# Optimization experiments

Measured on AMD Instinct MI355X. Metric: run time of the kernel, lower is better.

## Reference

```python
import jax, jax.numpy as jnp
import numpy as np

B, S, HID = 1, 2048, 2048
NH = 16
QL, KVL = 1536, 512
DN, DR, DV = 128, 64, 128
DQ = DN + DR  # 192
IH, ID = 4, 128
TOPK = 1024
EPS = 1e-6
THETA = 10000.0


def rope_interleaved(x, cos, sin):
    # x: (b,s,h,d); cos/sin: (s,d//2); pairs are (x[...,2i], x[...,2i+1])
    xr = x[..., 0::2]
    xi = x[..., 1::2]
    c = cos[None, :, None, :]
    s = sin[None, :, None, :]
    yr = xr * c - xi * s
    yi = xr * s + xi * c
    return jnp.stack([yr, yi], axis=-1).reshape(x.shape)


def rope_noninterleaved(x, cos, sin):
    # rotate-half style: pairs are (x[...,i], x[...,i+d/2])
    d = x.shape[-1] // 2
    x1, x2 = x[..., :d], x[..., d:]
    c = cos[None, :, None, :]
    s = sin[None, :, None, :]
    return jnp.concatenate([x1 * c - x2 * s, x1 * s + x2 * c], axis=-1)


def rmsnorm(x, w):
    var = jnp.mean(x * x, axis=-1, keepdims=True)
    return w * (x * jax.lax.rsqrt(var + EPS))


def layernorm(x, g, b):
    mu = jnp.mean(x, axis=-1, keepdims=True)
    var = jnp.mean((x - mu) ** 2, axis=-1, keepdims=True)
    return (x - mu) * jax.lax.rsqrt(var + EPS) * g + b


def setup_inputs() -> dict:
    key = jax.random.key(0)
    ks = jax.random.split(key, 12)
    std = 0.02
    x = jax.random.normal(ks[0], (B, S, HID), jnp.float32)
    pos = jnp.arange(S, dtype=jnp.float32)
    inv_freq = THETA ** (-jnp.arange(0, DR, 2, dtype=jnp.float32) / DR)
    ang = pos[:, None] * inv_freq[None, :]  # (S, DR//2)
    cos, sin = jnp.cos(ang), jnp.sin(ang)
    mask = jnp.where(jnp.tril(jnp.ones((S, S), bool)), 0.0, -1e9).astype(jnp.float32)
    return {
        "x": x, "cos": cos, "sin": sin, "mask": mask,
        "Wq_a": jax.random.normal(ks[1], (HID, QL), jnp.float32) * std,
        "q_norm_w": jnp.ones((QL,), jnp.float32),
        "Wq_b": jax.random.normal(ks[2], (QL, NH * DQ), jnp.float32) * std,
        "Wkv_a": jax.random.normal(ks[3], (HID, KVL + DR), jnp.float32) * std,
        "kv_norm_w": jnp.ones((KVL,), jnp.float32),
        "Wkv_b": jax.random.normal(ks[4], (KVL, NH * (DN + DV)), jnp.float32) * std,
        "Wo": jax.random.normal(ks[5], (NH * DV, HID), jnp.float32) * std,
        "IWq_b": jax.random.normal(ks[6], (QL, IH * ID), jnp.float32) * std,
        "IWk": jax.random.normal(ks[7], (HID, ID), jnp.float32) * std,
        "Ik_norm_w": jnp.ones((ID,), jnp.float32),
        "Ik_norm_b": jnp.zeros((ID,), jnp.float32),
        "IWproj": jax.random.normal(ks[8], (HID, IH), jnp.float32) * std,
    }


def indexer(x, qr, cos, sin, mask, IWq_b, IWk, Ik_norm_w, Ik_norm_b, IWproj):
    b, s, _ = x.shape
    q = (qr @ IWq_b).reshape(b, s, IH, ID)
    q_pe, q_nope = q[..., :DR], q[..., DR:]
    q_pe = rope_noninterleaved(q_pe, cos, sin)
    q = jnp.concatenate([q_pe, q_nope], axis=-1)
    k = layernorm(x @ IWk, Ik_norm_w, Ik_norm_b)  # (b,s,ID)
    k_pe = rope_noninterleaved(k[:, :, None, :DR], cos, sin)[:, :, 0]
    k = jnp.concatenate([k_pe, k[..., DR:]], axis=-1)
    weights = (x @ IWproj) * (IH ** -0.5) * (ID ** -0.5)  # (b,s,IH)
    logits = jax.nn.relu(jnp.einsum('bthd,bsd->btsh', q, k))
    index_score = jnp.einsum('btsh,bth->bts', logits, weights)
    index_score = index_score + mask[None]
    k_top = min(TOPK, s)
    topk_idx = jax.lax.top_k(index_score, k_top)[1]  # (b,s,k)
    bi = jnp.arange(b)[:, None, None]
    si = jnp.arange(s)[None, :, None]
    index_mask = jnp.full((b, s, s), -1e9, jnp.float32).at[bi, si, topk_idx].set(0.0)
    return index_mask


def reference(x, cos, sin, mask, Wq_a, q_norm_w, Wq_b, Wkv_a, kv_norm_w, Wkv_b, Wo,
              IWq_b, IWk, Ik_norm_w, Ik_norm_b, IWproj):
    b, s, _ = x.shape
    qr = rmsnorm(x @ Wq_a, q_norm_w)  # (b,s,QL)
    q = (qr @ Wq_b).reshape(b, s, NH, DQ)
    q_nope, q_pe = q[..., :DN], q[..., DN:]
    q_pe = rope_interleaved(q_pe, cos, sin)
    q = jnp.concatenate([q_nope, q_pe], axis=-1)
    kv_full = x @ Wkv_a
    kv, k_pe = kv_full[..., :KVL], kv_full[..., KVL:]
    kv = rmsnorm(kv, kv_norm_w)
    k_pe = rope_interleaved(k_pe[:, :, None, :], cos, sin)  # (b,s,1,DR)
    kv_exp = (kv @ Wkv_b).reshape(b, s, NH, DN + DV)
    k_nope, v = kv_exp[..., :DN], kv_exp[..., DN:]
    k = jnp.concatenate([k_nope, jnp.broadcast_to(k_pe, (b, s, NH, DR))], axis=-1)
    scores = jnp.einsum('bshd,bthd->bsht', q, k) * (DQ ** -0.5)
    index_mask = indexer(x, qr, cos, sin, mask, IWq_b, IWk, Ik_norm_w, Ik_norm_b, IWproj)
    scores = scores + index_mask[:, :, None, :] + mask[None, :, None, :]
    probs = jax.nn.softmax(scores, axis=-1)
    out = jnp.einsum('bsht,bthd->bshd', probs, v).reshape(b, s, NH * DV)
    return out @ Wo
```

## Files before the change

kernel.cpp:

```cpp
#include <hip/hip_runtime.h>
#include <math.h>
#include <stdint.h>

#define S 2048
#define HID 2048
#define NH 16
#define QL 1536
#define KVL 512
#define DN 128
#define DR 64
#define DV 128
#define DQ 192
#define IH 4
#define ID 128
#define TOPK 1024

#define N1 2244
#define N2 3584

#define WT_OFF3 ((size_t)N2 * QL)
#define WT_OFF4 (WT_OFF3 + (size_t)4096 * KVL)
#define WT_OFF5 (WT_OFF4 + (size_t)2048 * 2048)
#define WT_TOTAL (WT_OFF5 + (size_t)N1 * HID)

#define CDIV(a,b) (((a)+(b)-1)/(b))

typedef float f32x4 __attribute__((ext_vector_type(4)));
typedef short bf16x8 __attribute__((ext_vector_type(8)));

__device__ __forceinline__ ushort f2b(float f) {
    uint32_t u = __float_as_uint(f);
    u += 0x7fffu + ((u >> 16) & 1u);
    return (ushort)(u >> 16);
}

#define GLL16(g, l)                                                            \
    __builtin_amdgcn_global_load_lds(                                          \
        (const __attribute__((address_space(1))) void*)(g),                    \
        (__attribute__((address_space(3))) void*)(l), 16, 0, 0)

#define STG64T(k0, s)                                                          \
    {                                                                          \
        _Pragma("unroll")                                                      \
        for (int p = 0; p < 4; p++) {                                          \
            GLL16(pA[p] + (k0), As + (s) * 8192 + p * 2048 + doff);            \
            GLL16(pB[p] + (k0), Bs + (s) * 8192 + p * 2048 + doff);            \
        }                                                                      \
    }

template<int HALF>
__device__ __forceinline__ void gemm_tile(const ushort* __restrict__ A,
                                          const ushort* __restrict__ BT,
                                          void* __restrict__ Cv,
                                          int N, int K, int row0, int col0,
                                          ushort* As, ushort* Bs) {
    const int tid = threadIdx.x;
    const int w = tid >> 6, l = tid & 63;
    const int quad = l >> 4, lane = l & 15;
    const int wr = (w >> 1) * 64, wc = (w & 1) * 64;
    f32x4 acc[4][4];
#pragma unroll
    for (int i = 0; i < 4; i++)
#pragma unroll
        for (int j = 0; j < 4; j++) acc[i][j] = (f32x4)0.f;

    const int r32 = tid >> 3;
    const int csw = (((tid & 7) ^ (r32 & 7)) * 8);
    const ushort* pA[4];
    const ushort* pB[4];
#pragma unroll
    for (int p = 0; p < 4; p++) {
        pA[p] = A + (size_t)(row0 + p * 32 + r32) * K + csw;
        int bn = col0 + p * 32 + r32; if (bn > N - 1) bn = N - 1;
        pB[p] = BT + (size_t)bn * K + csw;
    }
    const int doff = r32 * 64 + (tid & 7) * 8;

    const int nt = K >> 6;
    STG64T(0, 0);
    asm volatile("s_waitcnt vmcnt(0)" ::: "memory");
    __builtin_amdgcn_s_barrier();

    const int xsw = (lane & 7) << 3;
    int cur = 0;
    for (int t = 0; t < nt; ++t) {
        if (t + 1 < nt) STG64T((t + 1) * 64, cur ^ 1);
#pragma unroll
        for (int kk = 0; kk < 2; kk++) {
            const int fo = (kk * 32 + quad * 8) ^ xsw;
            bf16x8 af[4], bf[4];
#pragma unroll
            for (int mi = 0; mi < 4; mi++)
                af[mi] = *(const bf16x8*)(As + cur * 8192 + (wr + mi * 16 + lane) * 64 + fo);
#pragma unroll
            for (int ni = 0; ni < 4; ni++)
                bf[ni] = *(const bf16x8*)(Bs + cur * 8192 + (wc + ni * 16 + lane) * 64 + fo);
#pragma unroll
            for (int mi = 0; mi < 4; mi++)
#pragma unroll
                for (int ni = 0; ni < 4; ni++)
                    acc[mi][ni] = __builtin_amdgcn_mfma_f32_16x16x32_bf16(af[mi], bf[ni], acc[mi][ni], 0, 0, 0);
        }
        asm volatile("s_waitcnt vmcnt(0)" ::: "memory");
        __builtin_amdgcn_s_barrier();
        cur ^= 1;
    }
#pragma unroll
    for (int mi = 0; mi < 4; mi++)
#pragma unroll
        for (int ni = 0; ni < 4; ni++)
#pragma unroll
            for (int r = 0; r < 4; r++) {
                int row = row0 + wr + mi * 16 + quad * 4 + r;
                int col = col0 + wc + ni * 16 + lane;
                if (col < N) {
                    if (HALF) ((ushort*)Cv)[(size_t)row * N + col] = f2b(acc[mi][ni][r]);
                    else      ((float*)Cv)[(size_t)row * N + col] = acc[mi][ni][r];
                }
            }
}

__device__ __forceinline__ void wtrans_lds(const float* W, ushort* WT, int K, int N,
                                           int k0, int n0, float* t) {
    int rr = threadIdx.x >> 6, cc = threadIdx.x & 63;
#pragma unroll
    for (int p = 0; p < 16; p++) {
        int k = k0 + p * 4 + rr, n = n0 + cc;
        t[(p * 4 + rr) * 65 + cc] = (k < K && n < N) ? W[(size_t)k * N + n] : 0.f;
    }
    __syncthreads();
#pragma unroll
    for (int p = 0; p < 16; p++) {
        int n = n0 + p * 4 + rr, k = k0 + cc;
        if (n < N && k < K) WT[(size_t)n * K + k] = f2b(t[cc * 65 + p * 4 + rr]);
    }
}

__global__ __launch_bounds__(256) void prep1(const float* __restrict__ x,
                                             ushort* __restrict__ xb,
                                             const float* __restrict__ W0,
                                             const float* __restrict__ W1,
                                             const float* __restrict__ W2,
                                             const float* __restrict__ W3,
                                             ushort* __restrict__ WTc1) {
    __shared__ float tb[64 * 65];
    const int id = blockIdx.x;
    if (id < 1152) {
        const float* W; int N; size_t off; int loc;
        if (id < 768)       { W = W0; N = 1536; off = 0;                  loc = id; }
        else if (id < 1056) { W = W1; N = 576;  off = (size_t)1536 * HID; loc = id - 768; }
        else if (id < 1120) { W = W2; N = 128;  off = (size_t)2112 * HID; loc = id - 1056; }
        else                { W = W3; N = 4;    off = (size_t)2240 * HID; loc = id - 1120; }
        wtrans_lds(W, WTc1 + off, HID, N, (loc & 31) * 64, (loc >> 5) * 64, tb);
    } else {
        const int i = (id - 1152) * 256 + threadIdx.x;
        float4 v = *(const float4*)(x + (size_t)i * 4);
        uint32_t lo = (uint32_t)f2b(v.x) | ((uint32_t)f2b(v.y) << 16);
        uint32_t hi = (uint32_t)f2b(v.z) | ((uint32_t)f2b(v.w) << 16);
        *(uint2*)(xb + (size_t)i * 4) = make_uint2(lo, hi);
    }
}

__global__ __launch_bounds__(256) void prep2(const float* __restrict__ W0,
                                             const float* __restrict__ W1,
                                             const float* __restrict__ Wkvb,
                                             const float* __restrict__ Wo,
                                             ushort* __restrict__ WT) {
    __shared__ float tb[64 * 65];
    const int id = blockIdx.x;
    const float* W; int K, N, nx; size_t off; int loc;
    if (id < 1152)      { W = W0;   K = QL;   N = 3072; nx = 24; off = 0;                 loc = id; }
    else if (id < 1344) { W = W1;   K = QL;   N = 512;  nx = 24; off = (size_t)3072 * QL; loc = id - 1152; }
    else if (id < 1856) { W = Wkvb; K = KVL;  N = 4096; nx = 8;  off = WT_OFF3;           loc = id - 1344; }
    else                { W = Wo;   K = 2048; N = 2048; nx = 32; off = WT_OFF4;           loc = id - 1856; }
    wtrans_lds(W, WT + off, K, N, (loc % nx) * 64, (loc / nx) * 64, tb);
}

__global__ __launch_bounds__(256) void gemm_f32(const ushort* __restrict__ A,
                                                const ushort* __restrict__ BT,
                                                float* __restrict__ C,
                                                int N, int K) {
    __shared__ ushort As[2][8192];
    __shared__ ushort Bs[2][8192];
    gemm_tile<0>(A, BT, C, N, K, blockIdx.y * 128, blockIdx.x * 128,
                 &As[0][0], &Bs[0][0]);
}

__global__ __launch_bounds__(256) void megaC2(const ushort* __restrict__ qrb,
                                              const ushort* __restrict__ kvnb,
                                              const ushort* __restrict__ WT,
                                              float* __restrict__ C2,
                                              ushort* __restrict__ kvexp_h) {
    __shared__ ushort As[2][8192];
    __shared__ ushort Bs[2][8192];
    const int id = blockIdx.x;
    if (id < 448) {
        gemm_tile<0>(qrb, WT, C2, N2, QL, (id / 28) * 128, (id % 28) * 128,
                     &As[0][0], &Bs[0][0]);
    } else {
        const int loc = id - 448;
        gemm_tile<1>(kvnb, WT + WT_OFF3, kvexp_h, 4096, KVL,
                     (loc / 32) * 128, (loc % 32) * 128, &As[0][0], &Bs[0][0]);
    }
}

__global__ __launch_bounds__(256) void post_c1(const float* __restrict__ C1,
                                               const float* __restrict__ qw,
                                               const float* __restrict__ kvw,
                                               const float* __restrict__ ikg,
                                               const float* __restrict__ ikb,
                                               const float* __restrict__ cosb,
                                               const float* __restrict__ sinb,
                                               ushort* __restrict__ qrb,
                                               ushort* __restrict__ kvnb,
                                               float* __restrict__ kpe,
                                               float* __restrict__ kiT) {
    const int t = blockIdx.x, tid = threadIdx.x;
    const float* row = C1 + (size_t)t * N1;
    __shared__ float red[256];
    __shared__ float kis[128];
    float ss = 0.f;
    for (int i = tid; i < 1536; i += 256) { float v = row[i]; ss += v * v; }
    red[tid] = ss; __syncthreads();
    for (int st = 128; st > 0; st >>= 1) { if (tid < st) red[tid] += red[tid + st]; __syncthreads(); }
    float sq = rsqrtf(red[0] / 1536.f + 1e-6f);
    __syncthreads();
    float s2 = 0.f;
    for (int i = tid; i < 512; i += 256) { float v = row[1536 + i]; s2 += v * v; }
    red[tid] = s2; __syncthreads();
    for (int st = 128; st > 0; st >>= 1) { if (tid < st) red[tid] += red[tid + st]; __syncthreads(); }
    float skv = rsqrtf(red[0] / 512.f + 1e-6f);
    __syncthreads();
    float kv_ = (tid < 128) ? row[2112 + tid] : 0.f;
    red[tid] = kv_; __syncthreads();
    for (int st = 128; st > 0; st >>= 1) { if (tid < st) red[tid] += red[tid + st]; __syncthreads(); }
    float mu = red[0] / 128.f;
    __syncthreads();
    red[tid] = kv_ * kv_; __syncthreads();
    for (int st = 128; st > 0; st >>= 1) { if (tid < st) red[tid] += red[tid + st]; __syncthreads(); }
    float var = red[0] / 128.f - mu * mu;
    for (int i = tid; i < 1536; i += 256) qrb[(size_t)t * QL + i] = f2b(row[i] * sq * qw[i]);
    for (int i = tid; i < 512; i += 256)  kvnb[(size_t)t * KVL + i] = f2b(row[1536 + i] * skv * kvw[i]);
    if (tid < 32) {
        float c = cosb[t * 32 + tid], s = sinb[t * 32 + tid];
        float xr = row[2048 + 2 * tid], xi = row[2048 + 2 * tid + 1];
        kpe[t * 64 + 2 * tid]     = xr * c - xi * s;
        kpe[t * 64 + 2 * tid + 1] = xr * s + xi * c;
    }
    if (tid < 128) kis[tid] = (kv_ - mu) * rsqrtf(var + 1e-6f) * ikg[tid] + ikb[tid];
    __syncthreads();
    if (tid < 128) {
        float outv;
        if (tid < 32) {
            float c = cosb[t * 32 + tid], s = sinb[t * 32 + tid];
            outv = kis[tid] * c - kis[tid + 32] * s;
        } else if (tid < 64) {
            int j = tid - 32;
            float c = cosb[t * 32 + j], s = sinb[t * 32 + j];
            outv = kis[j] * s + kis[tid] * c;
        } else {
            outv = kis[tid];
        }
        kiT[(size_t)tid * S + t] = outv;
    }
}

__global__ __launch_bounds__(256) void megaPost(float* __restrict__ C2,
                                                const float* __restrict__ cosb,
                                                const float* __restrict__ sinb,
                                                ushort* __restrict__ qb,
                                                const ushort* __restrict__ kvexp_h,
                                                const float* __restrict__ kpe,
                                                ushort* __restrict__ kb,
                                                ushort* __restrict__ vT) {
    __shared__ float cs[32], sn[32];
    __shared__ ushort tt[64][136];
    const int id = blockIdx.x, tid = threadIdx.x;
    if (id < 2048) {
        const int t = id;
        if (tid < 32) { cs[tid] = cosb[t * 32 + tid]; sn[tid] = sinb[t * 32 + tid]; }
        __syncthreads();
        const float sc = 0.10412775370051047f;
        const float* src0 = C2 + (size_t)t * N2;
        for (int i = tid; i < NH * 96; i += 256) {
            int h = i / 96, p = i % 96;
            const float* src = src0 + h * 192;
            ushort* dst = qb + ((size_t)h * S + t) * 192;
            if (p < 64) {
                dst[2 * p]     = f2b(src[2 * p] * sc);
                dst[2 * p + 1] = f2b(src[2 * p + 1] * sc);
            } else {
                int j = p - 64;
                float c = cs[j], s = sn[j];
                float xr = src[128 + 2 * j], xi = src[128 + 2 * j + 1];
                dst[128 + 2 * j]     = f2b((xr * c - xi * s) * sc);
                dst[128 + 2 * j + 1] = f2b((xr * s + xi * c) * sc);
            }
        }
        if (tid < 128) {
            int h = tid >> 5, j = tid & 31;
            float* p = C2 + (size_t)t * N2 + 3072 + h * 128;
            float c = cs[j], s = sn[j];
            float x1 = p[j], x2 = p[j + 32];
            p[j] = x1 * c - x2 * s;
            p[j + 32] = x1 * s + x2 * c;
        }
    } else {
        const int loc = id - 2048;
        const int s0 = (loc & 31) * 64, h = loc >> 5;
        const int row = tid >> 2, c = tid & 3;
        const ushort* src = kvexp_h + (size_t)(s0 + row) * 4096 + h * 256;
        ushort* kbr = kb + ((size_t)h * S + s0 + row) * 192;
#pragma unroll
        for (int i = 0; i < 4; i++) {
            int off = c * 32 + i * 8;
            *(uint4*)(kbr + off) = *(const uint4*)(src + off);
            *(uint4*)(&tt[row][off]) = *(const uint4*)(src + 128 + off);
        }
        const float* kp = kpe + (size_t)(s0 + row) * 64 + c * 16;
#pragma unroll
        for (int i = 0; i < 16; i++) kbr[128 + c * 16 + i] = f2b(kp[i]);
        __syncthreads();
        const int d = tid >> 1, sh = (tid & 1) * 32;
        ushort* dst = vT + ((size_t)h * 128 + d) * S + s0 + sh;
#pragma unroll
        for (int i = 0; i < 32; i++) dst[i] = tt[sh + i][d];
    }
}

__global__ __launch_bounds__(256) void iscore4x4(const float* __restrict__ qi,
                                                 const float* __restrict__ kiT,
                                                 const float* __restrict__ iw,
                                                 float* __restrict__ iscore) {
    const int t0 = blockIdx.x * 4;
    const int s0 = blockIdx.y * 1024;
    if (s0 > t0 + 3) return;
    const int s = s0 + threadIdx.x * 4;
    __shared__ float qsT[4 * ID * 4];
    __shared__ float ws[16];
    for (int i = threadIdx.x; i < 4 * ID * 4; i += 256) {
        int tt = i & 3, hd = i >> 2;
        qsT[hd * 4 + tt] = qi[(size_t)(t0 + tt) * N2 + hd];
    }
    if (threadIdx.x < 16) {
        int tt = threadIdx.x >> 2, h = threadIdx.x & 3;
        ws[threadIdx.x] = iw[(size_t)(t0 + tt) * N1 + h] * 0.04419417382415922f;
    }
    __syncthreads();
    if (s > t0 + 3) return;
    float a[4][4][4];
#pragma unroll
    for (int tt = 0; tt < 4; tt++)
#pragma unroll
        for (int h = 0; h < 4; h++)
#pragma unroll
            for (int c = 0; c < 4; c++) a[tt][h][c] = 0.f;
    for (int d = 0; d < ID; d++) {
        float4 kv = *(const float4*)(kiT + (size_t)d * S + s);
#pragma unroll
        for (int h = 0; h < 4; h++) {
            float4 qv = *(const float4*)(&qsT[(h * ID + d) * 4]);
            a[0][h][0] += qv.x * kv.x; a[0][h][1] += qv.x * kv.y;
            a[0][h][2] += qv.x * kv.z; a[0][h][3] += qv.x * kv.w;
            a[1][h][0] += qv.y * kv.x; a[1][h][1] += qv.y * kv.y;
            a[1][h][2] += qv.y * kv.z; a[1][h][3] += qv.y * kv.w;
            a[2][h][0] += qv.z * kv.x; a[2][h][1] += qv.z * kv.y;
            a[2][h][2] += qv.z * kv.z; a[2][h][3] += qv.z * kv.w;
            a[3][h][0] += qv.w * kv.x; a[3][h][1] += qv.w * kv.y;
            a[3][h][2] += qv.w * kv.z; a[3][h][3] += qv.w * kv.w;
        }
    }
#pragma unroll
    for (int tt = 0; tt < 4; tt++) {
        const int t = t0 + tt;
        if (s > t) continue;
#pragma unroll
        for (int c = 0; c < 4; c++) {
            if (s + c > t) break;
            float sc = fmaxf(a[tt][0][c], 0.f) * ws[tt * 4 + 0] +
                       fmaxf(a[tt][1][c], 0.f) * ws[tt * 4 + 1] +
                       fmaxf(a[tt][2][c], 0.f) * ws[tt * 4 + 2] +
                       fmaxf(a[tt][3][c], 0.f) * ws[tt * 4 + 3];
            iscore[(size_t)t * S + s + c] = sc;
        }
    }
}

__device__ inline unsigned sortable_u32(float f) {
    unsigned u = __float_as_uint(f);
    return (u & 0x80000000u) ? ~u : (u | 0x80000000u);
}

__global__ __launch_bounds__(256) void topk_mask(const float* __restrict__ iscore,
                                                 uint32_t* __restrict__ msk) {
    int t = blockIdx.x, tid = threadIdx.x;
    uint32_t* mrow = msk + (size_t)t * 64;
    if (t < TOPK) {
        if (tid < 64) {
            int full = (t + 1) >> 5;
            uint32_t wv2 = (tid < full) ? 0xFFFFFFFFu : 0u;
            if (tid == full) { int rem = (t + 1) & 31; wv2 = rem ? ((1u << rem) - 1u) : 0u; }
            mrow[tid] = wv2;
        }
        return;
    }
    const float* row = iscore + (size_t)t * S;
    const int n = t + 1;
    const int wv = tid >> 6, lane = tid & 63;
    __shared__ int hist[4][256];
    __shared__ int wtot[4];
    __shared__ int bsel, ksel;
    __shared__ uint32_t bytes[256];

    int jb = tid * 8;
    float4 v0 = *(const float4*)(row + jb);
    float4 v1 = *(const float4*)(row + jb + 4);
    uint32_t lsu[8];
    {
        float vvv[8] = {v0.x, v0.y, v0.z, v0.w, v1.x, v1.y, v1.z, v1.w};
#pragma unroll
        for (int i = 0; i < 8; i++)
            lsu[i] = (jb + i < n) ? sortable_u32(vvv[i]) : 0u;
    }
    unsigned prefix = 0, prefmask = 0;
    int k = TOPK;
    for (int pass = 0; pass < 4; pass++) {
        int shift = 24 - pass * 8;
#pragma unroll
        for (int r = 0; r < 4; r++) hist[r][tid] = 0;
        __syncthreads();
#pragma unroll
        for (int i = 0; i < 8; i++) {
            uint32_t u = lsu[i];
            if ((u & prefmask) == prefix) atomicAdd(&hist[wv][(u >> shift) & 255], 1);
        }
        __syncthreads();
        int h = hist[0][tid] + hist[1][tid] + hist[2][tid] + hist[3][tid];
        int x = h;
#pragma unroll
        for (int off = 1; off < 64; off <<= 1) {
            int tmp = __shfl_down(x, off, 64);
            if (lane + off < 64) x += tmp;
        }
        if (lane == 0) wtot[wv] = x;
        __syncthreads();
        int add = 0;
#pragma unroll
        for (int w2 = 1; w2 < 4; w2++) if (w2 > wv) add += wtot[w2];
        x += add;
        int snext = x - h;
        if (x >= k && snext < k) { bsel = tid; ksel = k - snext; }
        __syncthreads();
        prefix |= ((unsigned)bsel) << shift;
        prefmask |= 0xFFu << shift;
        k = ksel;
        __syncthreads();
    }
    const unsigned u_thr = prefix;
    const int need = k;
    uint32_t gtbits = 0, eqbits = 0;
    int eqcnt = 0;
#pragma unroll
    for (int i = 0; i < 8; i++) {
        uint32_t u = lsu[i];
        if (u > u_thr) gtbits |= 1u << i;
        else if (u == u_thr) { eqbits |= 1u << i; eqcnt++; }
    }
    {
        int x = eqcnt;
#pragma unroll
        for (int off = 1; off < 64; off <<= 1) {
            int tmp = __shfl_up(x, off, 64);
            if (lane >= off) x += tmp;
        }
        if (lane == 63) wtot[wv] = x;
        __syncthreads();
        int add = 0;
#pragma unroll
        for (int w2 = 0; w2 < 3; w2++) if (w2 < wv) add += wtot[w2];
        x += add;
        int room = need - (x - eqcnt);
        uint32_t keep = 0;
#pragma unroll
        for (int i = 0; i < 8; i++)
            if ((eqbits >> i) & 1u) { if (room > 0) { keep |= 1u << i; room--; } }
        bytes[tid] = gtbits | keep;
    }
    __syncthreads();
    if (tid < 64)
        mrow[tid] = bytes[tid * 4] | (bytes[tid * 4 + 1] << 8) |
                    (bytes[tid * 4 + 2] << 16) | (bytes[tid * 4 + 3] << 24);
}

__global__ __launch_bounds__(256, 2) void fattn10(const ushort* __restrict__ qb,
                                                  const ushort* __restrict__ kb,
                                                  const ushort* __restrict__ vT,
                                                  const uint32_t* __restrict__ msk,
                                                  float* __restrict__ Opart,
                                                  float* __restrict__ mlbuf) {
    __shared__ ushort Ks[24 * 512];
    __shared__ ushort Vs[16 * 512];
    __shared__ ushort Pm[4][16 * 72];
    const int tid = threadIdx.x;
    const int w = tid >> 6, l = tid & 63, quad = l >> 4, lane = l & 15;
    const int b = blockIdx.x;
    const int r8 = b & 7, j = b >> 3;
    const int h = r8 + 8 * (j & 1);
    const int idx = j >> 1;
    const int pair = idx & 15, part = idx >> 4;
    const int ta = pair, tb = 31 - pair, nA = ta + 1;
    const int vlo = part * 11, vhi = vlo + 11;
    const int qa0 = ta * 64, qb0 = tb * 64;

    bf16x8 qfa[6], qfb[6];
    {
        const ushort* qpa = qb + ((size_t)h * S + qa0 + w * 16 + lane) * 192;
        const ushort* qpb = qb + ((size_t)h * S + qb0 + w * 16 + lane) * 192;
#pragma unroll
        for (int ks = 0; ks < 6; ks++) {
            qfa[ks] = *(const bf16x8*)(qpa + ks * 32 + quad * 8);
            qfb[ks] = *(const bf16x8*)(qpb + ks * 32 + quad * 8);
        }
    }
    f32x4 oa[8], ob[8];
#pragma unroll
    for (int i = 0; i < 8; i++) { oa[i] = (f32x4)0.f; ob[i] = (f32x4)0.f; }
    float la[4], lb[4];
#pragma unroll
    for (int r = 0; r < 4; r++) { la[r] = 0.f; lb[r] = 0.f; }

    ushort* pw = &Pm[w][0];
    const ushort* kbase = kb + (size_t)h * S * 192;
    const ushort* vbase = vT + (size_t)h * 128 * S;

    for (int kt = 0; kt <= tb; kt++) {
        const int idxB = (kt <= ta) ? 2 * kt : kt + nA;
        const int hasA = (kt <= ta);
        const int idxA = 2 * kt + 1;
        const bool doB = (idxB >= vlo && idxB < vhi);
        const bool doA = hasA && (idxA >= vlo && idxA < vhi);
        if (!(doA || doB)) continue;
        const int s0 = kt * 64;
        __syncthreads();
#pragma unroll
        for (int ii = 0; ii < 6; ii++) {
            const int i = w * 6 + ii;
            const int ks = i >> 2, kq = i & 3;
            const ushort* src = kbase + (size_t)(s0 + kq * 16 + lane) * 192 + ks * 32 + quad * 8;
            GLL16(src, Ks + i * 512 + l * 8);
        }
#pragma unroll
        for (int ii = 0; ii < 4; ii++) {
            const int i = w * 4 + ii;
            const int k2 = i >> 3, nt = i & 7;
            const ushort* src = vbase + (size_t)(nt * 16 + lane) * S + s0 + k2 * 32 + quad * 8;
            GLL16(src, Vs + i * 512 + l * 8);
        }
        __syncthreads();

#pragma unroll
        for (int pass = 0; pass < 2; pass++) {
            if (pass == 0 && !doA) continue;
            if (pass == 1 && !doB) continue;
            const bf16x8* qf = (pass == 0) ? qfa : qfb;
            f32x4* oacc      = (pass == 0) ? oa : ob;
            float* ll        = (pass == 0) ? la : lb;
            const int q0t    = (pass == 0) ? qa0 : qb0;

            f32x4 sc[4];
#pragma unroll
            for (int kq = 0; kq < 4; kq++) {
                sc[kq] = (f32x4)0.f;
#pragma unroll
                for (int ks = 0; ks < 6; ks++) {
                    bf16x8 bfr = *(const bf16x8*)(Ks + (ks * 4 + kq) * 512 + quad * 128 + lane * 8);
                    sc[kq] = __builtin_amdgcn_mfma_f32_16x16x32_bf16(qf[ks], bfr, sc[kq], 0, 0, 0);
                }
            }
            uint32_t w0[4], w1[4];
            {
                const int rowbase = q0t + w * 16 + quad * 4;
#pragma unroll
                for (int r = 0; r < 4; r++) {
                    const uint32_t* mp = msk + (size_t)(rowbase + r) * 64 + (s0 >> 5);
                    w0[r] = mp[0]; w1[r] = mp[1];
                }
            }
#pragma unroll
            for (int kq = 0; kq < 4; kq++) {
                const int sh = (kq & 1) * 16 + lane;
#pragma unroll
                for (int r = 0; r < 4; r++) {
                    uint32_t word = (kq < 2) ? w0[r] : w1[r];
                    float v = ((word >> sh) & 1u) ? sc[kq][r] : -1e30f;
                    float e = exp2f(v);
                    ll[r] += e;
                    pw[(quad * 4 + r) * 72 + kq * 16 + lane] = f2b(e);
                }
            }

            bf16x8 pfr[2];
#pragma unroll
            for (int k2 = 0; k2 < 2; k2++)
                pfr[k2] = *(const bf16x8*)(pw + lane * 72 + k2 * 32 + quad * 8);
#pragma unroll
            for (int nt = 0; nt < 8; nt++) {
#pragma unroll
                for (int k2 = 0; k2 < 2; k2++) {
                    bf16x8 vfr = *(const bf16x8*)(Vs + ((k2 * 8 + nt) * 4 + quad) * 128 + lane * 8);
                    oacc[nt] = __builtin_amdgcn_mfma_f32_16x16x32_bf16(pfr[k2], vfr, oacc[nt], 0, 0, 0);
                }
            }
        }
    }
#pragma unroll
    for (int off = 1; off < 16; off <<= 1)
#pragma unroll
        for (int r = 0; r < 4; r++) {
            la[r] += __shfl_xor(la[r], off, 64);
            lb[r] += __shfl_xor(lb[r], off, 64);
        }
#pragma unroll
    for (int pass = 0; pass < 2; pass++) {
        const f32x4* oacc = (pass == 0) ? oa : ob;
        const float* ll   = (pass == 0) ? la : lb;
        const int qt      = (pass == 0) ? ta : tb;
        float* Op = Opart + (size_t)((qt * 16 + h) * 3 + part) * (64 * 128);
        float* mlp = mlbuf + (size_t)((qt * 16 + h) * 3 + part) * 128;
#pragma unroll
        for (int nt = 0; nt < 8; nt++)
#pragma unroll
            for (int r = 0; r < 4; r++)
                Op[(w * 16 + quad * 4 + r) * 128 + nt * 16 + lane] = oacc[nt][r];
        if (lane == 0) {
#pragma unroll
            for (int r = 0; r < 4; r++) {
                mlp[(w * 16 + quad * 4 + r) * 2 + 0] = 0.f;
                mlp[(w * 16 + quad * 4 + r) * 2 + 1] = ll[r];
            }
        }
    }
}

__global__ __launch_bounds__(256) void attn_combine(const float* __restrict__ Opart,
                                                    const float* __restrict__ mlbuf,
                                                    ushort* __restrict__ attn_b) {
    const int qt = blockIdx.x, h = blockIdx.y, tid = threadIdx.x;
    const size_t base = ((size_t)qt * 16 + h) * 3;
    const float* Op0 = Opart + base * 8192;
    const float* Op1 = Op0 + 8192;
    const float* Op2 = Op1 + 8192;
    const float* ml0 = mlbuf + base * 128;
    const float* ml1 = ml0 + 128;
    const float* ml2 = ml1 + 128;
#pragma unroll
    for (int i = 0; i < 32; i++) {
        int id = tid + i * 256;
        int row = id >> 7, d = id & 127;
        float m0 = ml0[row * 2], l0 = ml0[row * 2 + 1];
        float m1 = ml1[row * 2], l1 = ml1[row * 2 + 1];
        float m2 = ml2[row * 2], l2 = ml2[row * 2 + 1];
        float m = fmaxf(fmaxf(m0, m1), m2);
        float e0 = exp2f(m0 - m), e1 = exp2f(m1 - m), e2 = exp2f(m2 - m);
        float linv = 1.f / (l0 * e0 + l1 * e1 + l2 * e2);
        float v = (Op0[id] * e0 + Op1[id] * e1 + Op2[id] * e2) * linv;
        attn_b[(size_t)(qt * 64 + row) * 2048 + h * 128 + d] = f2b(v);
    }
}

extern "C" void kernel_launch(void* const* d_in, const int* in_sizes, int n_in,
                              void* d_out, int out_size, void* d_ws, size_t ws_size,
                              hipStream_t stream) {
    const float* x        = (const float*)d_in[0];
    const float* cosb     = (const float*)d_in[1];
    const float* sinb     = (const float*)d_in[2];
    const float* Wq_a     = (const float*)d_in[4];
    const float* q_norm_w = (const float*)d_in[5];
    const float* Wq_b     = (const float*)d_in[6];
    const float* Wkv_a    = (const float*)d_in[7];
    const float* kv_norm_w= (const float*)d_in[8];
    const float* Wkv_b    = (const float*)d_in[9];
    const float* Wo       = (const float*)d_in[10];
    const float* IWq_b    = (const float*)d_in[11];
    const float* IWk      = (const float*)d_in[12];
    const float* Ik_norm_w= (const float*)d_in[13];
    const float* Ik_norm_b= (const float*)d_in[14];
    const float* IWproj   = (const float*)d_in[15];
    float* out = (float*)d_out;

    char* ws = (char*)d_ws;
    size_t o = 0;
    auto take = [&](size_t b) { char* p = ws + o; o += (b + 255) & ~(size_t)255; return p; };
    ushort* xb     = (ushort*)take((size_t)S * HID * 2);
    ushort* qrb    = (ushort*)take((size_t)S * QL * 2);
    ushort* qb     = (ushort*)take((size_t)NH * S * DQ * 2);
    ushort* kvnb   = (ushort*)take((size_t)S * KVL * 2);
    float*  kpe    = (float*)take((size_t)S * DR * 4);
    ushort* kb     = (ushort*)take((size_t)NH * S * DQ * 2);
    ushort* vT     = (ushort*)take((size_t)NH * DV * S * 2);
    uint32_t* msk  = (uint32_t*)take((size_t)S * 64 * 4);
    float*  mlbuf  = (float*)take((size_t)32 * 16 * 3 * 64 * 2 * 4);
    ushort* WTp    = (ushort*)take(WT_TOTAL * 2);
    float*  C1     = (float*)take((size_t)S * N1 * 4);
    char*   big    = take((size_t)32 * 16 * 3 * 8192 * 4 + 1024);
    ushort* kvexp_h= (ushort*)take((size_t)S * 4096 * 2);
    float*  kiT    = (float*)take((size_t)128 * S * 4);
    char*   poolb  = take((size_t)16777216);

    float* C2     = (float*)big;
    float* Opart  = (float*)big;
    float* iscore = (float*)poolb;
    ushort* attn_b = (ushort*)poolb;

    prep1<<<5248, 256, 0, stream>>>(x, xb, Wq_a, Wkv_a, IWk, IWproj, WTp + WT_OFF5);

    gemm_f32<<<dim3(CDIV(N1, 128), S / 128), 256, 0, stream>>>(xb, WTp + WT_OFF5, C1, N1, HID);
    prep2<<<2880, 256, 0, stream>>>(Wq_b, IWq_b, Wkv_b, Wo, WTp);
    post_c1<<<S, 256, 0, stream>>>(C1, q_norm_w, kv_norm_w, Ik_norm_w, Ik_norm_b,
                                   cosb, sinb, qrb, kvnb, kpe, kiT);

    megaC2<<<960, 256, 0, stream>>>(qrb, kvnb, WTp, C2, kvexp_h);

    megaPost<<<2560, 256, 0, stream>>>(C2, cosb, sinb, qb, kvexp_h, kpe, kb, vT);

    iscore4x4<<<dim3(S / 4, S / 1024), 256, 0, stream>>>(C2 + 3072, kiT, C1 + 2240, iscore);
    topk_mask<<<S, 256, 0, stream>>>(iscore, msk);

    fattn10<<<768, 256, 0, stream>>>(qb, kb, vT, msk, Opart, mlbuf);
    attn_combine<<<dim3(32, 16), 256, 0, stream>>>(Opart, mlbuf, attn_b);

    gemm_f32<<<dim3(HID / 128, S / 128), 256, 0, stream>>>(attn_b, WTp + WT_OFF4, out, HID, NH * DV);

    (void)in_sizes; (void)n_in; (void)out_size; (void)ws_size; (void)o;
}
```

Measured before the change: 462.7 us.

## Merge weight-prep kernels and compute indexer scores only for rows beyond TOPK

Combines the two weight-transpose/convert kernels into one launch, so the second transpose set is no longer a separate dispatch between the first GEMM and post_c1. The indexer score kernel now launches only for query rows t >= TOPK, since rows with at most TOPK causal keys select every key regardless of score. This relies on topk_mask handling those early rows without reading their scores, which the diff does not show. It also drops the early-exit guard because s0 <= t0 always holds for the remaining rows.

```diff
diff --git a/kernel.cpp b/kernel.cpp
--- a/kernel.cpp
+++ b/kernel.cpp
@@ -136,44 +136,41 @@
     }
 }
 
-__global__ __launch_bounds__(256) void prep1(const float* __restrict__ x,
-                                             ushort* __restrict__ xb,
-                                             const float* __restrict__ W0,
-                                             const float* __restrict__ W1,
-                                             const float* __restrict__ W2,
-                                             const float* __restrict__ W3,
-                                             ushort* __restrict__ WTc1) {
+__global__ __launch_bounds__(256) void prepAll(const float* __restrict__ x,
+                                               ushort* __restrict__ xb,
+                                               const float* __restrict__ Wq_a,
+                                               const float* __restrict__ Wkv_a,
+                                               const float* __restrict__ IWk,
+                                               const float* __restrict__ IWproj,
+                                               const float* __restrict__ Wq_b,
+                                               const float* __restrict__ IWq_b,
+                                               const float* __restrict__ Wkvb,
+                                               const float* __restrict__ Wo,
+                                               ushort* __restrict__ WT) {
     __shared__ float tb[64 * 65];
     const int id = blockIdx.x;
     if (id < 1152) {
         const float* W; int N; size_t off; int loc;
-        if (id < 768)       { W = W0; N = 1536; off = 0;                  loc = id; }
-        else if (id < 1056) { W = W1; N = 576;  off = (size_t)1536 * HID; loc = id - 768; }
-        else if (id < 1120) { W = W2; N = 128;  off = (size_t)2112 * HID; loc = id - 1056; }
-        else                { W = W3; N = 4;    off = (size_t)2240 * HID; loc = id - 1120; }
-        wtrans_lds(W, WTc1 + off, HID, N, (loc & 31) * 64, (loc >> 5) * 64, tb);
-    } else {
+        if (id < 768)       { W = Wq_a;   N = 1536; off = 0;                  loc = id; }
+        else if (id < 1056) { W = Wkv_a;  N = 576;  off = (size_t)1536 * HID; loc = id - 768; }
+        else if (id < 1120) { W = IWk;    N = 128;  off = (size_t)2112 * HID; loc = id - 1056; }
+        else                { W = IWproj; N = 4;    off = (size_t)2240 * HID; loc = id - 1120; }
+        wtrans_lds(W, WT + WT_OFF5 + off, HID, N, (loc & 31) * 64, (loc >> 5) * 64, tb);
+    } else if (id < 5248) {
         const int i = (id - 1152) * 256 + threadIdx.x;
         float4 v = *(const float4*)(x + (size_t)i * 4);
         uint32_t lo = (uint32_t)f2b(v.x) | ((uint32_t)f2b(v.y) << 16);
         uint32_t hi = (uint32_t)f2b(v.z) | ((uint32_t)f2b(v.w) << 16);
         *(uint2*)(xb + (size_t)i * 4) = make_uint2(lo, hi);
-    }
-}
-
-__global__ __launch_bounds__(256) void prep2(const float* __restrict__ W0,
-                                             const float* __restrict__ W1,
-                                             const float* __restrict__ Wkvb,
-                                             const float* __restrict__ Wo,
-                                             ushort* __restrict__ WT) {
-    __shared__ float tb[64 * 65];
-    const int id = blockIdx.x;
-    const float* W; int K, N, nx; size_t off; int loc;
-    if (id < 1152)      { W = W0;   K = QL;   N = 3072; nx = 24; off = 0;                 loc = id; }
-    else if (id < 1344) { W = W1;   K = QL;   N = 512;  nx = 24; off = (size_t)3072 * QL; loc = id - 1152; }
-    else if (id < 1856) { W = Wkvb; K = KVL;  N = 4096; nx = 8;  off = WT_OFF3;           loc = id - 1344; }
-    else                { W = Wo;   K = 2048; N = 2048; nx = 32; off = WT_OFF4;           loc = id - 1856; }
-    wtrans_lds(W, WT + off, K, N, (loc % nx) * 64, (loc / nx) * 64, tb);
+    } else {
+        const int pid = id - 5248;
+        const float* W; int K, N, nx; size_t off; int loc;
+        if (pid < 1152)      { W = Wq_b;  K = QL;   N = 3072; nx = 24; off = 0;                 loc = pid; }
+        else if (pid < 1344) { W = IWq_b; K = QL;   N = 512;  nx = 24; off = (size_t)3072 * QL; loc = pid - 1152; }
+        else if (pid < 1856) { W = Wkvb;  K = KVL;  N = 4096; nx = 8;  off = WT_OFF3;           loc = pid - 1344; }
+        else                 { W = Wo;    K = 2048; N = 2048; nx = 32; off = WT_OFF4;           loc = pid - 1856; }
+        wtrans_lds(W, WT + off, K, N, (loc % nx) * 64, (loc / nx) * 64, tb);
+    }
 }
 
 __global__ __launch_bounds__(256) void gemm_f32(const ushort* __restrict__ A,
@@ -332,9 +329,8 @@
                                                  const float* __restrict__ kiT,
                                                  const float* __restrict__ iw,
                                                  float* __restrict__ iscore) {
-    const int t0 = blockIdx.x * 4;
+    const int t0 = TOPK + blockIdx.x * 4;
     const int s0 = blockIdx.y * 1024;
-    if (s0 > t0 + 3) return;
     const int s = s0 + threadIdx.x * 4;
     __shared__ float qsT[4 * ID * 4];
     __shared__ float ws[16];
@@ -712,10 +708,10 @@
     float* iscore = (float*)poolb;
     ushort* attn_b = (ushort*)poolb;
 
-    prep1<<<5248, 256, 0, stream>>>(x, xb, Wq_a, Wkv_a, IWk, IWproj, WTp + WT_OFF5);
+    prepAll<<<8128, 256, 0, stream>>>(x, xb, Wq_a, Wkv_a, IWk, IWproj,
+                                      Wq_b, IWq_b, Wkv_b, Wo, WTp);
 
     gemm_f32<<<dim3(CDIV(N1, 128), S / 128), 256, 0, stream>>>(xb, WTp + WT_OFF5, C1, N1, HID);
-    prep2<<<2880, 256, 0, stream>>>(Wq_b, IWq_b, Wkv_b, Wo, WTp);
     post_c1<<<S, 256, 0, stream>>>(C1, q_norm_w, kv_norm_w, Ik_norm_w, Ik_norm_b,
                                    cosb, sinb, qrb, kvnb, kpe, kiT);
 
@@ -723,7 +719,7 @@
 
     megaPost<<<2560, 256, 0, stream>>>(C2, cosb, sinb, qb, kvexp_h, kpe, kb, vT);
 
-    iscore4x4<<<dim3(S / 4, S / 1024), 256, 0, stream>>>(C2 + 3072, kiT, C1 + 2240, iscore);
+    iscore4x4<<<dim3(256, 2), 256, 0, stream>>>(C2 + 3072, kiT, C1 + 2240, iscore);
     topk_mask<<<S, 256, 0, stream>>>(iscore, msk);
 
     fattn10<<<768, 256, 0, stream>>>(qb, kb, vT, msk, Opart, mlbuf);
```

Result: no change. 454.2 us (-1.8%).
